# Performance work log

Hardware: AMD Instinct MI355X
Metric: run time of the kernel (lower is better)

Reference implementation:

```python
import jax, jax.numpy as jnp
import numpy as np

NUM_ITERATIONS = 3
NUM_ROUTES = 6912  # 32*6*6*6


def _squash(t):
    # t: [..., O]; squash along last dim
    sq = jnp.sum(t * t, axis=-1, keepdims=True)
    return sq * t / ((1.0 + sq) * jnp.sqrt(sq))


def setup_inputs() -> dict:
    key = jax.random.key(0)
    k1, k2 = jax.random.split(key)
    B, R, I, C, O = 64, NUM_ROUTES, 8, 10, 16
    x = jax.random.normal(k1, (B, R, I), dtype=jnp.float32)
    route_weights = jax.random.normal(k2, (C, R, I, O), dtype=jnp.float32)
    return {"x": x, "route_weights": route_weights}


def reference(x, route_weights):
    # x: [B, R, I]; route_weights: [C, R, I, O]
    # priors = x[None,:,:,None,:] @ W[:,None,:,:,:] -> [C, B, R, 1, O]
    priors = jnp.einsum('bri,crio->cbro', x, route_weights)[:, :, :, None, :]
    logits = jnp.zeros_like(priors)  # [C, B, R, 1, O]
    outputs = None
    for i in range(NUM_ITERATIONS):
        # softmax over routes (dim=2), matching custom softmax(input, dim=2)
        probs = jax.nn.softmax(logits, axis=2)
        outputs = _squash(jnp.sum(probs * priors, axis=2, keepdims=True))  # [C,B,1,1,O]
        if i != NUM_ROUTES - 1:  # always true in original (num_routes >> iters)
            delta = jnp.sum(priors * outputs, axis=-1, keepdims=True)  # [C,B,R,1,1]
            logits = logits + delta
    return outputs
```

## Files before the change

### kernel.cpp

```cpp
#include <hip/hip_runtime.h>
#include <math.h>

#define BB 64
#define RR 6912
#define II 8
#define CC 10
#define OO 16
#define RPB 64
#define NCH 108
#define NIT 8
#define LDSF 4608

typedef _Float16 h2 __attribute__((ext_vector_type(2)));
union HV { int4 v; h2 h[4]; };

__global__ __launch_bounds__(256) void transpose_cvt_kernel(
    const float* __restrict__ x, int4* __restrict__ xth4)
{
    __shared__ float4 lds4[64 * 34];
    const int rblk = blockIdx.x >> 2;
    const int bblk = blockIdx.x & 3;
    const int r0 = rblk * 64, b0 = bblk * 16;
    const int t = threadIdx.x;
    {
        const int rl = t & 63;
        const int bl0 = t >> 6;
#pragma unroll
        for (int kb = 0; kb < 4; ++kb) {
            const int bl = kb * 4 + bl0;
            const float4* src = (const float4*)(x + ((size_t)(b0 + bl) * RR + (r0 + rl)) * II);
            lds4[rl * 34 + bl * 2 + 0] = src[0];
            lds4[rl * 34 + bl * 2 + 1] = src[1];
        }
    }
    __syncthreads();
    {
        const int bl = t & 15;
        const int rw0 = t >> 4;
#pragma unroll
        for (int kr = 0; kr < 4; ++kr) {
            const int rw = kr * 16 + rw0;
            float4 a = lds4[rw * 34 + bl * 2 + 0];
            float4 bq = lds4[rw * 34 + bl * 2 + 1];
            HV u;
            u.h[0] = h2{(_Float16)a.x,  (_Float16)a.y};
            u.h[1] = h2{(_Float16)a.z,  (_Float16)a.w};
            u.h[2] = h2{(_Float16)bq.x, (_Float16)bq.y};
            u.h[3] = h2{(_Float16)bq.z, (_Float16)bq.w};
            xth4[(size_t)(r0 + rw) * BB + (b0 + bl)] = u.v;
        }
    }
}

__global__ __launch_bounds__(256) void wcvt_kernel(
    const float4* __restrict__ w4, int4* __restrict__ wh4)
{
    __shared__ __align__(16) _Float16 wl[1024];
    const int blk = blockIdx.x;
    const int t = threadIdx.x;
    const float4 v = w4[(size_t)blk * 256 + t];
    const int rp = t >> 5;
    const int i  = (t >> 2) & 7;
    const int o0 = (t & 3) * 4;
    wl[(rp * 16 + o0 + 0) * 8 + i] = (_Float16)v.x;
    wl[(rp * 16 + o0 + 1) * 8 + i] = (_Float16)v.y;
    wl[(rp * 16 + o0 + 2) * 8 + i] = (_Float16)v.z;
    wl[(rp * 16 + o0 + 3) * 8 + i] = (_Float16)v.w;
    __syncthreads();
    if (t < 128) wh4[(size_t)blk * 128 + t] = ((const int4*)wl)[t];
}

template <int MODE>
__global__ __launch_bounds__(256, 4) void pass_kernel(
    const int4* __restrict__ xth4, const int4* __restrict__ wh4,
    const float* __restrict__ ov_in,
    float* __restrict__ pacc, float* __restrict__ pz)
{
    __shared__ __align__(16) float lds[LDSF];
    int4* wlds = (int4*)lds;

    const int bid = blockIdx.x;
    const int c = bid / NCH;
    const int chunk = bid - c * NCH;
    const int t = threadIdx.x;
    const int wv = t >> 6;
    const int lane = t & 63;
    const int rr = lane >> 5;
    const int bg = lane & 31;

    {
        const int4* src = wh4 + (size_t)(c * (RR / 8) + chunk * 8) * 128;
#pragma unroll
        for (int k = 0; k < 4; ++k) wlds[k * 256 + t] = src[k * 256 + t];
    }

    float acc0[OO], acc1[OO];
#pragma unroll
    for (int o = 0; o < OO; ++o) { acc0[o] = 0.f; acc1[o] = 0.f; }
    float Z0 = 0.f, Z1 = 0.f;

    float ov0[OO], ov1[OO];
    if (MODE != 0) {
        const float4* opa = (const float4*)(ov_in + ((size_t)c * BB + bg) * OO);
        const float4* opb = (const float4*)(ov_in + ((size_t)c * BB + bg + 32) * OO);
#pragma unroll
        for (int q = 0; q < 4; ++q) {
            float4 va = opa[q], vb = opb[q];
            ov0[q*4+0]=va.x; ov0[q*4+1]=va.y; ov0[q*4+2]=va.z; ov0[q*4+3]=va.w;
            ov1[q*4+0]=vb.x; ov1[q*4+1]=vb.y; ov1[q*4+2]=vb.z; ov1[q*4+3]=vb.w;
        }
    }

    __syncthreads();

#pragma unroll 1
    for (int it = 0; it < NIT; ++it) {
        const int rl = it * 8 + wv * 2 + rr;
        const int r  = chunk * RPB + rl;
        HV xa, xb;
        xa.v = xth4[(size_t)r * BB + bg];
        xb.v = xth4[(size_t)r * BB + bg + 32];

        float p0[OO], p1[OO];
#pragma unroll
        for (int o = 0; o < OO; ++o) {
            HV wq; wq.v = wlds[rl * 16 + o];
            float a = __builtin_amdgcn_fdot2(xa.h[0], wq.h[0],
                        (MODE == 0) ? acc0[o] : 0.f, false);
            a = __builtin_amdgcn_fdot2(xa.h[1], wq.h[1], a, false);
            a = __builtin_amdgcn_fdot2(xa.h[2], wq.h[2], a, false);
            a = __builtin_amdgcn_fdot2(xa.h[3], wq.h[3], a, false);
            float bb = __builtin_amdgcn_fdot2(xb.h[0], wq.h[0],
                        (MODE == 0) ? acc1[o] : 0.f, false);
            bb = __builtin_amdgcn_fdot2(xb.h[1], wq.h[1], bb, false);
            bb = __builtin_amdgcn_fdot2(xb.h[2], wq.h[2], bb, false);
            bb = __builtin_amdgcn_fdot2(xb.h[3], wq.h[3], bb, false);
            if (MODE == 0) { acc0[o] = a; acc1[o] = bb; }
            else           { p0[o] = a;   p1[o] = bb; }
        }

        if (MODE != 0) {
            float d0 = 0.f, d1 = 0.f;
#pragma unroll
            for (int o = 0; o < OO; ++o) { d0 = fmaf(p0[o], ov0[o], d0); d1 = fmaf(p1[o], ov1[o], d1); }
            const float e0 = __expf(d0), e1 = __expf(d1);
            Z0 += e0; Z1 += e1;
#pragma unroll
            for (int o = 0; o < OO; ++o) { acc0[o] = fmaf(e0, p0[o], acc0[o]); acc1[o] = fmaf(e1, p1[o], acc1[o]); }
        }
    }

#pragma unroll
    for (int o = 0; o < OO; ++o) {
        acc0[o] += __shfl_xor(acc0[o], 32);
        acc1[o] += __shfl_xor(acc1[o], 32);
    }
    if (MODE != 0) { Z0 += __shfl_xor(Z0, 32); Z1 += __shfl_xor(Z1, 32); }

    __syncthreads();
    if (rr == 0) {
        float* s = lds + (wv * 32 + bg) * 36;
#pragma unroll
        for (int o = 0; o < OO; ++o) { s[o] = acc0[o]; s[16 + o] = acc1[o]; }
        s[32] = Z0; s[33] = Z1;
    }
    __syncthreads();

    {
        const int b = t >> 2, q = t & 3;
        const int k = b >> 5, bgf = b & 31;
        float4 sum = make_float4(0.f, 0.f, 0.f, 0.f);
#pragma unroll
        for (int w2 = 0; w2 < 4; ++w2) {
            const float4 v = *(const float4*)(lds + (w2 * 32 + bgf) * 36 + k * 16 + q * 4);
            sum.x += v.x; sum.y += v.y; sum.z += v.z; sum.w += v.w;
        }
        *(float4*)(pacc + (((size_t)(c * NCH + chunk) * BB + b) * OO) + q * 4) = sum;
        if (MODE != 0 && q == 0) {
            float z = 0.f;
#pragma unroll
            for (int w2 = 0; w2 < 4; ++w2) z += lds[(w2 * 32 + bgf) * 36 + 32 + k];
            pz[(size_t)(c * NCH + chunk) * BB + b] = z;
        }
    }
}

template <int MODE>
__global__ __launch_bounds__(256) void combine_kernel(
    const float* __restrict__ pacc, const float* __restrict__ pz,
    const float* __restrict__ out0, float* __restrict__ outw)
{
    __shared__ float lsum[256];
    __shared__ float lz[16];
    const int cb = blockIdx.x;
    const int c = cb >> 6, b = cb & 63;
    const int t = threadIdx.x;
    const int o = t & 15, g = t >> 4;

    float s = 0.f, zl = 0.f;
    for (int p = g; p < NCH; p += 16) {
        s += pacc[((size_t)(c * NCH + p) * BB + b) * OO + o];
        if (MODE != 0 && o == 0) zl += pz[(size_t)(c * NCH + p) * BB + b];
    }
    lsum[t] = s;
    if (MODE != 0 && o == 0) lz[g] = zl;
    __syncthreads();

    if (g == 0) {
#pragma unroll
        for (int k = 1; k < 16; ++k) s += lsum[k * 16 + o];
        if (MODE != 0) {
            float Zt = 0.f;
#pragma unroll
            for (int k = 0; k < 16; ++k) Zt += lz[k];
            s /= Zt;
        } else {
            s *= (1.0f / RR);
        }
        float sq = s * s;
#pragma unroll
        for (int w = 1; w < 16; w <<= 1) sq += __shfl_xor(sq, w);
        float val = s * sqrtf(sq) / (1.f + sq);
        if (MODE == 1) val += out0[(size_t)cb * OO + o];
        outw[(size_t)cb * OO + o] = val;
    }
}

extern "C" void kernel_launch(void* const* d_in, const int* in_sizes, int n_in,
                              void* d_out, int out_size, void* d_ws, size_t ws_size,
                              hipStream_t stream)
{
    const float* x = (const float*)d_in[0];
    const float* w = (const float*)d_in[1];
    float* out = (float*)d_out;

    float* ws = (float*)d_ws;
    float* xth    = ws;
    float* wh     = xth + (size_t)RR * BB * 4;
    float* pacc   = wh + (size_t)CC * RR * 64;
    float* pz     = pacc + (size_t)CC * NCH * BB * OO;
    float* out0   = pz + (size_t)CC * NCH * BB;
    float* outsum = out0 + CC * BB * OO;

    int4* xth4 = (int4*)xth;
    int4* wh4  = (int4*)wh;
    const float4* w4 = (const float4*)w;

    transpose_cvt_kernel<<<dim3((RR / 64) * 4), dim3(256), 0, stream>>>(x, xth4);
    wcvt_kernel<<<dim3(CC * (RR / 8)), dim3(256), 0, stream>>>(w4, wh4);

    const dim3 gp(CC * NCH), bp(256);
    const dim3 gc(CC * BB), bc(256);

    pass_kernel<0><<<gp, bp, 0, stream>>>(xth4, wh4, nullptr, pacc, pz);
    combine_kernel<0><<<gc, bc, 0, stream>>>(pacc, pz, nullptr, out0);
    pass_kernel<1><<<gp, bp, 0, stream>>>(xth4, wh4, out0, pacc, pz);
    combine_kernel<1><<<gc, bc, 0, stream>>>(pacc, pz, out0, outsum);
    pass_kernel<2><<<gp, bp, 0, stream>>>(xth4, wh4, outsum, pacc, pz);
    combine_kernel<2><<<gc, bc, 0, stream>>>(pacc, pz, nullptr, out);
}
```

Before: 166.9 us.

## Fuse conversion prepasses and combine step into pass kernels via last-block reduction

Drops the separate x-transpose and weight-conversion kernels: pass 0 converts its own weight slice to fp16 in LDS and writes it out for later passes, and every pass reads x in fp32 directly and packs it to fp16 with round-toward-zero conversion. The combine kernels are replaced by an atomic counter per capsule, so the last finishing block reduces the partials and applies squash. This cuts the launch count from eight to three plus a memset and removes the xth intermediate buffer. In exchange, x is read with strided uncoalesced accesses three times, the final reduction runs serially in one block per capsule, and round-toward-zero conversion slightly changes numerics.

```diff
diff --git a/kernel.cpp b/kernel.cpp
--- a/kernel.cpp
+++ b/kernel.cpp
@@ -9,74 +9,27 @@
 #define RPB 64
 #define NCH 108
 #define NIT 8
+#define GRID (CC * NCH)
 #define LDSF 4608
 
 typedef _Float16 h2 __attribute__((ext_vector_type(2)));
+typedef __fp16  g2 __attribute__((ext_vector_type(2)));
 union HV { int4 v; h2 h[4]; };
 
-__global__ __launch_bounds__(256) void transpose_cvt_kernel(
-    const float* __restrict__ x, int4* __restrict__ xth4)
-{
-    __shared__ float4 lds4[64 * 34];
-    const int rblk = blockIdx.x >> 2;
-    const int bblk = blockIdx.x & 3;
-    const int r0 = rblk * 64, b0 = bblk * 16;
-    const int t = threadIdx.x;
-    {
-        const int rl = t & 63;
-        const int bl0 = t >> 6;
-#pragma unroll
-        for (int kb = 0; kb < 4; ++kb) {
-            const int bl = kb * 4 + bl0;
-            const float4* src = (const float4*)(x + ((size_t)(b0 + bl) * RR + (r0 + rl)) * II);
-            lds4[rl * 34 + bl * 2 + 0] = src[0];
-            lds4[rl * 34 + bl * 2 + 1] = src[1];
-        }
-    }
-    __syncthreads();
-    {
-        const int bl = t & 15;
-        const int rw0 = t >> 4;
-#pragma unroll
-        for (int kr = 0; kr < 4; ++kr) {
-            const int rw = kr * 16 + rw0;
-            float4 a = lds4[rw * 34 + bl * 2 + 0];
-            float4 bq = lds4[rw * 34 + bl * 2 + 1];
-            HV u;
-            u.h[0] = h2{(_Float16)a.x,  (_Float16)a.y};
-            u.h[1] = h2{(_Float16)a.z,  (_Float16)a.w};
-            u.h[2] = h2{(_Float16)bq.x, (_Float16)bq.y};
-            u.h[3] = h2{(_Float16)bq.z, (_Float16)bq.w};
-            xth4[(size_t)(r0 + rw) * BB + (b0 + bl)] = u.v;
-        }
-    }
-}
-
-__global__ __launch_bounds__(256) void wcvt_kernel(
-    const float4* __restrict__ w4, int4* __restrict__ wh4)
-{
-    __shared__ __align__(16) _Float16 wl[1024];
-    const int blk = blockIdx.x;
-    const int t = threadIdx.x;
-    const float4 v = w4[(size_t)blk * 256 + t];
-    const int rp = t >> 5;
-    const int i  = (t >> 2) & 7;
-    const int o0 = (t & 3) * 4;
-    wl[(rp * 16 + o0 + 0) * 8 + i] = (_Float16)v.x;
-    wl[(rp * 16 + o0 + 1) * 8 + i] = (_Float16)v.y;
-    wl[(rp * 16 + o0 + 2) * 8 + i] = (_Float16)v.z;
-    wl[(rp * 16 + o0 + 3) * 8 + i] = (_Float16)v.w;
-    __syncthreads();
-    if (t < 128) wh4[(size_t)blk * 128 + t] = ((const int4*)wl)[t];
+static __device__ __forceinline__ h2 pkrtz(float a, float b) {
+    g2 r = __builtin_amdgcn_cvt_pkrtz(a, b);
+    return __builtin_bit_cast(h2, r);
 }
 
 template <int MODE>
 __global__ __launch_bounds__(256, 4) void pass_kernel(
-    const int4* __restrict__ xth4, const int4* __restrict__ wh4,
-    const float* __restrict__ ov_in,
-    float* __restrict__ pacc, float* __restrict__ pz)
+    const float* __restrict__ x, const float4* __restrict__ w4,
+    int4* __restrict__ wh4, const float* __restrict__ ov_in,
+    float* __restrict__ pacc, float* __restrict__ pz,
+    int* __restrict__ cnt, float* __restrict__ outw)
 {
     __shared__ __align__(16) float lds[LDSF];
+    __shared__ int lastflag;
     int4* wlds = (int4*)lds;
 
     const int bid = blockIdx.x;
@@ -88,16 +41,28 @@
     const int rr = lane >> 5;
     const int bg = lane & 31;
 
-    {
-        const int4* src = wh4 + (size_t)(c * (RR / 8) + chunk * 8) * 128;
+    if (MODE == 0) {
+        _Float16* wl = (_Float16*)lds;
+        const int rp = t >> 5, i = (t >> 2) & 7, o0 = (t & 3) * 4;
+        const float4* src = w4 + (size_t)(c * RR + chunk * RPB) * 32;
+#pragma unroll 1
+        for (int k = 0; k < 8; ++k) {
+            const float4 v = src[k * 256 + t];
+            const int rl8 = k * 8 + rp;
+            wl[(rl8 * 16 + o0 + 0) * 8 + i] = (_Float16)v.x;
+            wl[(rl8 * 16 + o0 + 1) * 8 + i] = (_Float16)v.y;
+            wl[(rl8 * 16 + o0 + 2) * 8 + i] = (_Float16)v.z;
+            wl[(rl8 * 16 + o0 + 3) * 8 + i] = (_Float16)v.w;
+        }
+        __syncthreads();
+        int4* dst = wh4 + (size_t)bid * 1024;
+#pragma unroll
+        for (int j = 0; j < 4; ++j) dst[j * 256 + t] = wlds[j * 256 + t];
+    } else {
+        const int4* src = wh4 + (size_t)bid * 1024;
 #pragma unroll
         for (int k = 0; k < 4; ++k) wlds[k * 256 + t] = src[k * 256 + t];
     }
-
-    float acc0[OO], acc1[OO];
-#pragma unroll
-    for (int o = 0; o < OO; ++o) { acc0[o] = 0.f; acc1[o] = 0.f; }
-    float Z0 = 0.f, Z1 = 0.f;
 
     float ov0[OO], ov1[OO];
     if (MODE != 0) {
@@ -113,13 +78,28 @@
 
     __syncthreads();
 
+    float acc0[OO], acc1[OO];
+#pragma unroll
+    for (int o = 0; o < OO; ++o) { acc0[o] = 0.f; acc1[o] = 0.f; }
+    float Z0 = 0.f, Z1 = 0.f;
+
 #pragma unroll 1
     for (int it = 0; it < NIT; ++it) {
         const int rl = it * 8 + wv * 2 + rr;
         const int r  = chunk * RPB + rl;
+        const float4* xp0 = (const float4*)(x + ((size_t)bg * RR + r) * II);
+        const float4* xp1 = (const float4*)(x + ((size_t)(bg + 32) * RR + r) * II);
+        const float4 a0 = xp0[0], a1 = xp0[1];
+        const float4 c0 = xp1[0], c1 = xp1[1];
         HV xa, xb;
-        xa.v = xth4[(size_t)r * BB + bg];
-        xb.v = xth4[(size_t)r * BB + bg + 32];
+        xa.h[0] = pkrtz(a0.x, a0.y);
+        xa.h[1] = pkrtz(a0.z, a0.w);
+        xa.h[2] = pkrtz(a1.x, a1.y);
+        xa.h[3] = pkrtz(a1.z, a1.w);
+        xb.h[0] = pkrtz(c0.x, c0.y);
+        xb.h[1] = pkrtz(c0.z, c0.w);
+        xb.h[2] = pkrtz(c1.x, c1.y);
+        xb.h[3] = pkrtz(c1.z, c1.w);
 
         float p0[OO], p1[OO];
 #pragma unroll
@@ -130,13 +110,13 @@
             a = __builtin_amdgcn_fdot2(xa.h[1], wq.h[1], a, false);
             a = __builtin_amdgcn_fdot2(xa.h[2], wq.h[2], a, false);
             a = __builtin_amdgcn_fdot2(xa.h[3], wq.h[3], a, false);
-            float bb = __builtin_amdgcn_fdot2(xb.h[0], wq.h[0],
+            float b2 = __builtin_amdgcn_fdot2(xb.h[0], wq.h[0],
                         (MODE == 0) ? acc1[o] : 0.f, false);
-            bb = __builtin_amdgcn_fdot2(xb.h[1], wq.h[1], bb, false);
-            bb = __builtin_amdgcn_fdot2(xb.h[2], wq.h[2], bb, false);
-            bb = __builtin_amdgcn_fdot2(xb.h[3], wq.h[3], bb, false);
-            if (MODE == 0) { acc0[o] = a; acc1[o] = bb; }
-            else           { p0[o] = a;   p1[o] = bb; }
+            b2 = __builtin_amdgcn_fdot2(xb.h[1], wq.h[1], b2, false);
+            b2 = __builtin_amdgcn_fdot2(xb.h[2], wq.h[2], b2, false);
+            b2 = __builtin_amdgcn_fdot2(xb.h[3], wq.h[3], b2, false);
+            if (MODE == 0) { acc0[o] = a; acc1[o] = b2; }
+            else           { p0[o] = a;   p1[o] = b2; }
         }
 
         if (MODE != 0) {
@@ -175,54 +155,49 @@
             const float4 v = *(const float4*)(lds + (w2 * 32 + bgf) * 36 + k * 16 + q * 4);
             sum.x += v.x; sum.y += v.y; sum.z += v.z; sum.w += v.w;
         }
-        *(float4*)(pacc + (((size_t)(c * NCH + chunk) * BB + b) * OO) + q * 4) = sum;
+        *(float4*)(pacc + ((size_t)bid * BB + b) * OO + q * 4) = sum;
         if (MODE != 0 && q == 0) {
             float z = 0.f;
 #pragma unroll
             for (int w2 = 0; w2 < 4; ++w2) z += lds[(w2 * 32 + bgf) * 36 + 32 + k];
-            pz[(size_t)(c * NCH + chunk) * BB + b] = z;
-        }
-    }
-}
-
-template <int MODE>
-__global__ __launch_bounds__(256) void combine_kernel(
-    const float* __restrict__ pacc, const float* __restrict__ pz,
-    const float* __restrict__ out0, float* __restrict__ outw)
-{
-    __shared__ float lsum[256];
-    __shared__ float lz[16];
-    const int cb = blockIdx.x;
-    const int c = cb >> 6, b = cb & 63;
-    const int t = threadIdx.x;
-    const int o = t & 15, g = t >> 4;
-
-    float s = 0.f, zl = 0.f;
-    for (int p = g; p < NCH; p += 16) {
-        s += pacc[((size_t)(c * NCH + p) * BB + b) * OO + o];
-        if (MODE != 0 && o == 0) zl += pz[(size_t)(c * NCH + p) * BB + b];
-    }
-    lsum[t] = s;
-    if (MODE != 0 && o == 0) lz[g] = zl;
-    __syncthreads();
-
-    if (g == 0) {
-#pragma unroll
-        for (int k = 1; k < 16; ++k) s += lsum[k * 16 + o];
+            pz[(size_t)bid * BB + b] = z;
+        }
+    }
+
+    __threadfence();
+    __syncthreads();
+    if (t == 0) lastflag = (atomicAdd(cnt + c, 1) == NCH - 1) ? 1 : 0;
+    __syncthreads();
+    if (lastflag) {
+        __threadfence();
+        const int b = t >> 2, q = t & 3;
+        float s0 = 0.f, s1 = 0.f, s2 = 0.f, s3 = 0.f, z = 0.f;
+#pragma unroll 4
+        for (int p = 0; p < NCH; ++p) {
+            const float4 v = *(const float4*)(pacc + ((size_t)(c * NCH + p) * BB + b) * OO + q * 4);
+            s0 += v.x; s1 += v.y; s2 += v.z; s3 += v.w;
+            if (MODE != 0) { if (q == 0) z += pz[(size_t)(c * NCH + p) * BB + b]; }
+        }
         if (MODE != 0) {
-            float Zt = 0.f;
-#pragma unroll
-            for (int k = 0; k < 16; ++k) Zt += lz[k];
-            s /= Zt;
+            float* zb = lds;
+            if (q == 0) zb[b] = z;
+            __syncthreads();
+            const float inv = 1.0f / zb[b];
+            s0 *= inv; s1 *= inv; s2 *= inv; s3 *= inv;
         } else {
-            s *= (1.0f / RR);
-        }
-        float sq = s * s;
-#pragma unroll
-        for (int w = 1; w < 16; w <<= 1) sq += __shfl_xor(sq, w);
-        float val = s * sqrtf(sq) / (1.f + sq);
-        if (MODE == 1) val += out0[(size_t)cb * OO + o];
-        outw[(size_t)cb * OO + o] = val;
+            const float inv = 1.0f / RR;
+            s0 *= inv; s1 *= inv; s2 *= inv; s3 *= inv;
+        }
+        float sq = s0 * s0 + s1 * s1 + s2 * s2 + s3 * s3;
+        sq += __shfl_xor(sq, 1);
+        sq += __shfl_xor(sq, 2);
+        const float f = sqrtf(sq) / (1.f + sq);
+        float4 val = make_float4(s0 * f, s1 * f, s2 * f, s3 * f);
+        if (MODE == 1) {
+            const float4 o4 = *(const float4*)(ov_in + ((size_t)c * BB + b) * OO + q * 4);
+            val.x += o4.x; val.y += o4.y; val.z += o4.z; val.w += o4.w;
+        }
+        *(float4*)(outw + ((size_t)c * BB + b) * OO + q * 4) = val;
     }
 }
 
@@ -231,31 +206,23 @@
                               hipStream_t stream)
 {
     const float* x = (const float*)d_in[0];
-    const float* w = (const float*)d_in[1];
+    const float4* w4 = (const float4*)d_in[1];
     float* out = (float*)d_out;
 
     float* ws = (float*)d_ws;
-    float* xth    = ws;
-    float* wh     = xth + (size_t)RR * BB * 4;
+    float* wh     = ws;
     float* pacc   = wh + (size_t)CC * RR * 64;
-    float* pz     = pacc + (size_t)CC * NCH * BB * OO;
-    float* out0   = pz + (size_t)CC * NCH * BB;
+    float* pz     = pacc + (size_t)GRID * BB * OO;
+    float* out0   = pz + (size_t)GRID * BB;
     float* outsum = out0 + CC * BB * OO;
-
-    int4* xth4 = (int4*)xth;
-    int4* wh4  = (int4*)wh;
-    const float4* w4 = (const float4*)w;
-
-    transpose_cvt_kernel<<<dim3((RR / 64) * 4), dim3(256), 0, stream>>>(x, xth4);
-    wcvt_kernel<<<dim3(CC * (RR / 8)), dim3(256), 0, stream>>>(w4, wh4);
-
-    const dim3 gp(CC * NCH), bp(256);
-    const dim3 gc(CC * BB), bc(256);
-
-    pass_kernel<0><<<gp, bp, 0, stream>>>(xth4, wh4, nullptr, pacc, pz);
-    combine_kernel<0><<<gc, bc, 0, stream>>>(pacc, pz, nullptr, out0);
-    pass_kernel<1><<<gp, bp, 0, stream>>>(xth4, wh4, out0, pacc, pz);
-    combine_kernel<1><<<gc, bc, 0, stream>>>(pacc, pz, out0, outsum);
-    pass_kernel<2><<<gp, bp, 0, stream>>>(xth4, wh4, outsum, pacc, pz);
-    combine_kernel<2><<<gc, bc, 0, stream>>>(pacc, pz, nullptr, out);
+    int*   cnt    = (int*)(outsum + CC * BB * OO);
+
+    int4* wh4 = (int4*)wh;
+
+    (void)hipMemsetAsync(cnt, 0, 3 * CC * sizeof(int), stream);
+
+    const dim3 gp(GRID), bp(256);
+    pass_kernel<0><<<gp, bp, 0, stream>>>(x, w4, wh4, nullptr, pacc, pz, cnt,          out0);
+    pass_kernel<1><<<gp, bp, 0, stream>>>(x, w4, wh4, out0,    pacc, pz, cnt + CC,     outsum);
+    pass_kernel<2><<<gp, bp, 0, stream>>>(x, w4, wh4, outsum,  pacc, pz, cnt + 2 * CC, out);
 }
```

Measured after the change: 509.2 us. 3.05x slower.
